# Kernel optimization log

Measured on AMD Instinct MI355X. Metric: run time of the kernel, lower is better.

The kernel has to match this reference:

```python
import jax, jax.numpy as jnp
import numpy as np

HIDDEN = 1024
N_HEAD = 16
D_HEAD = HIDDEN // N_HEAD


def setup_inputs() -> dict:
    key = jax.random.key(0)
    ks = jax.random.split(key, 12)
    B, S, H = 2, 2048, HIDDEN
    scale = 1.0 / np.sqrt(H)
    inp = {
        "q": jax.random.normal(ks[0], (B, S, H), jnp.float32),
        "k": jax.random.normal(ks[1], (B, S, H), jnp.float32),
        "v": jax.random.normal(ks[2], (B, S, H), jnp.float32),
        "mask": jnp.ones((B, 1, S, S), jnp.int32),
        "w_q": jax.random.normal(ks[3], (H, H), jnp.float32) * scale,
        "b_q": jnp.zeros((H,), jnp.float32),
        "w_k": jax.random.normal(ks[4], (H, H), jnp.float32) * scale,
        "b_k": jnp.zeros((H,), jnp.float32),
        "w_v": jax.random.normal(ks[5], (H, H), jnp.float32) * scale,
        "b_v": jnp.zeros((H,), jnp.float32),
        "w_o": jax.random.normal(ks[6], (H, H), jnp.float32) * scale,
        "b_o": jnp.zeros((H,), jnp.float32),
    }
    return inp


def reference(q, k, v, mask, w_q, b_q, w_k, b_k, w_v, b_v, w_o, b_o):
    B, Sq, H = q.shape
    Sk = k.shape[1]
    # projections (weights stored as [in, out])
    qh = (q @ w_q + b_q).reshape(B, Sq, N_HEAD, D_HEAD).transpose(0, 2, 1, 3)
    kh = (k @ w_k + b_k).reshape(B, Sk, N_HEAD, D_HEAD).transpose(0, 2, 1, 3)
    vh = (v @ w_v + b_v).reshape(B, Sk, N_HEAD, D_HEAD).transpose(0, 2, 1, 3)
    scores = jnp.einsum("bhqd,bhkd->bhqk", qh, kh) * (D_HEAD ** -0.5)
    scores = jnp.where(mask == 0, jnp.float32(-10000.0), scores)
    attn = jax.nn.softmax(scores, axis=-1)
    out = jnp.einsum("bhqk,bhkd->bhqd", attn, vh)
    out = out.transpose(0, 2, 1, 3).reshape(B, Sq, H)
    return out @ w_o + b_o
```

## Files before the change

kernel.cpp:

```cpp
#include <hip/hip_runtime.h>
#include <hip/hip_bf16.h>
#include <stdint.h>

#define S_LEN 2048
#define HID   1024
#define NHEAD 16
#define DHEAD 64
#define BATCH 2

#define QSCALE 0.18033688f
#define MASKNEG -14427.0f

typedef __bf16 bf16_t;
typedef __bf16 bf16x4 __attribute__((ext_vector_type(4)));
typedef __bf16 bf16x8 __attribute__((ext_vector_type(8)));
typedef float  f32x4  __attribute__((ext_vector_type(4)));

__device__ __forceinline__ void gl_lds16(const bf16_t* g, bf16_t* l) {
  __builtin_amdgcn_global_load_lds((const __attribute__((address_space(1))) void*)g,
                                   (__attribute__((address_space(3))) void*)l,
                                   16, 0, 0);
}

template<int TR, int TC>
__device__ __forceinline__ void stage_tile(const bf16_t* __restrict__ g, int ldg,
                                           bf16_t* lds, int wave, int lane) {
  constexpr int CH = TC / 8;
  constexpr int NINST = (TR * CH) / 64;
  #pragma unroll
  for (int i = wave; i < NINST; i += 4) {
    int slot = i * 64 + lane;
    int r  = slot / CH;
    int cs = slot & (CH - 1);
    int c  = cs ^ (r & (CH - 1));
    gl_lds16(g + (size_t)r * ldg + c * 8, lds + i * 512);
  }
}

template<int CH>
__device__ __forceinline__ bf16x8 frag_ld(const bf16_t* lds, int row, int kchunk) {
  int cs = kchunk ^ (row & (CH - 1));
  return *(const bf16x8*)(lds + (row * CH + cs) * 8);
}

__global__ __launch_bounds__(256) void cvt3(const float* __restrict__ q,
                                            const float* __restrict__ k,
                                            const float* __restrict__ v,
                                            bf16_t* __restrict__ qb,
                                            bf16_t* __restrict__ kb,
                                            bf16_t* __restrict__ vb) {
  int which = blockIdx.y;
  const float* src = which == 0 ? q : which == 1 ? k : v;
  bf16_t* dst = which == 0 ? qb : which == 1 ? kb : vb;
  size_t i = ((size_t)blockIdx.x * 256 + threadIdx.x) * 4;
  float4 u = *(const float4*)(src + i);
  bf16x4 o = {(bf16_t)u.x, (bf16_t)u.y, (bf16_t)u.z, (bf16_t)u.w};
  *(bf16x4*)(dst + i) = o;
}

__global__ __launch_bounds__(256) void transpose_w4(
    const float* __restrict__ w0, const float* __restrict__ w1,
    const float* __restrict__ w2, const float* __restrict__ w3,
    bf16_t* __restrict__ wt) {
  __shared__ float t[64][65];
  const float* W = blockIdx.z == 0 ? w0 : blockIdx.z == 1 ? w1 : blockIdx.z == 2 ? w2 : w3;
  bf16_t* WT = wt + (size_t)blockIdx.z * HID * HID;
  int tx = threadIdx.x & 63, ty = threadIdx.x >> 6;
  int r0 = blockIdx.y * 64, c0 = blockIdx.x * 64;
  #pragma unroll
  for (int i = ty; i < 64; i += 4) t[i][tx] = W[(size_t)(r0 + i) * HID + c0 + tx];
  __syncthreads();
  #pragma unroll
  for (int i = ty; i < 64; i += 4) WT[(size_t)(c0 + i) * HID + r0 + tx] = (bf16_t)t[tx][i];
}

__global__ __launch_bounds__(256) void mask_flags(const int* __restrict__ mask,
                                                  unsigned char* __restrict__ flags) {
  int kt = blockIdx.x, qtile = blockIdx.y, b = blockIdx.z;
  const int* base = mask + (size_t)b * S_LEN * S_LEN + (size_t)(qtile * 128) * S_LEN + kt * 128;
  int tid = threadIdx.x;
  int r = tid >> 1, half = tid & 1;
  const int4* p = (const int4*)(base + (size_t)r * S_LEN + half * 64);
  int ok = 1;
  #pragma unroll
  for (int i = 0; i < 16; ++i) {
    int4 u = p[i];
    ok &= (u.x != 0) & (u.y != 0) & (u.z != 0) & (u.w != 0);
  }
  __shared__ int anyz;
  if (tid == 0) anyz = 0;
  __syncthreads();
  if (!ok) atomicOr(&anyz, 1);
  __syncthreads();
  if (tid == 0) flags[(b * 16 + qtile) * 16 + kt] = anyz ? 0 : 1;
}

__global__ __launch_bounds__(256) void qkv_gemm(
    const bf16_t* __restrict__ qb, const bf16_t* __restrict__ kb, const bf16_t* __restrict__ vb,
    const bf16_t* __restrict__ wT,
    const float* __restrict__ bq, const float* __restrict__ bk, const float* __restrict__ bv,
    bf16_t* __restrict__ Qh, bf16_t* __restrict__ Kh, bf16_t* __restrict__ VhT) {
  int mode = blockIdx.z;
  const bf16_t* A    = mode == 0 ? qb : mode == 1 ? kb : vb;
  const bf16_t* Bt   = wT + (size_t)mode * HID * HID;
  const float*  bias = mode == 0 ? bq : mode == 1 ? bk : bv;

  __shared__ __align__(16) bf16_t As[128 * 64];
  __shared__ __align__(16) bf16_t Bs[128 * 64];

  int tid = threadIdx.x, wave = tid >> 6, lane = tid & 63;
  int lane15 = lane & 15, quad = lane >> 4;
  int m0 = blockIdx.x * 128, n0 = blockIdx.y * 128;
  int wm = (wave >> 1) * 64, wn = (wave & 1) * 64;

  f32x4 zero4 = {0.f, 0.f, 0.f, 0.f};
  f32x4 acc[4][4];
  #pragma unroll
  for (int t = 0; t < 4; ++t)
    #pragma unroll
    for (int n = 0; n < 4; ++n) acc[t][n] = zero4;

  for (int k0 = 0; k0 < HID; k0 += 64) {
    stage_tile<128, 64>(A  + (size_t)m0 * HID + k0, HID, As, wave, lane);
    stage_tile<128, 64>(Bt + (size_t)n0 * HID + k0, HID, Bs, wave, lane);
    __syncthreads();
    #pragma unroll
    for (int kc = 0; kc < 2; ++kc) {
      bf16x8 af[4], bfr[4];
      #pragma unroll
      for (int t = 0; t < 4; ++t) af[t]  = frag_ld<8>(As, wm + t * 16 + lane15, kc * 4 + quad);
      #pragma unroll
      for (int n = 0; n < 4; ++n) bfr[n] = frag_ld<8>(Bs, wn + n * 16 + lane15, kc * 4 + quad);
      if (mode < 2) {
        #pragma unroll
        for (int t = 0; t < 4; ++t)
          #pragma unroll
          for (int n = 0; n < 4; ++n)
            acc[t][n] = __builtin_amdgcn_mfma_f32_16x16x32_bf16(af[t], bfr[n], acc[t][n], 0, 0, 0);
      } else {
        #pragma unroll
        for (int t = 0; t < 4; ++t)
          #pragma unroll
          for (int n = 0; n < 4; ++n)
            acc[t][n] = __builtin_amdgcn_mfma_f32_16x16x32_bf16(bfr[n], af[t], acc[t][n], 0, 0, 0);
      }
    }
    __syncthreads();
  }

  if (mode < 2) {
    float sc = (mode == 0) ? QSCALE : 1.0f;
    bf16_t* dst = (mode == 0 ? Qh : Kh);
    #pragma unroll
    for (int t = 0; t < 4; ++t) {
      #pragma unroll
      for (int n = 0; n < 4; ++n) {
        int col = n0 + wn + n * 16 + lane15;
        float bb = bias[col];
        #pragma unroll
        for (int i = 0; i < 4; ++i) {
          int row = m0 + wm + t * 16 + quad * 4 + i;
          bf16_t o = (bf16_t)((acc[t][n][i] + bb) * sc);
          int b = row >> 11, s = row & 2047;
          int h = col >> 6,  d = col & 63;
          dst[((size_t)(b * NHEAD + h) * S_LEN + s) * DHEAD + d] = o;
        }
      }
    }
  } else {
    #pragma unroll
    for (int n = 0; n < 4; ++n) {
      int dbase = n0 + wn + n * 16 + quad * 4;
      float4 bb4 = *(const float4*)(bias + dbase);
      #pragma unroll
      for (int t = 0; t < 4; ++t) {
        int token = m0 + wm + t * 16 + lane15;
        int b = token >> 11, s = token & 2047;
        #pragma unroll
        for (int i = 0; i < 4; ++i) {
          int dg = dbase + i;
          int h = dg >> 6, d = dg & 63;
          float bb = i == 0 ? bb4.x : i == 1 ? bb4.y : i == 2 ? bb4.z : bb4.w;
          VhT[((size_t)(b * NHEAD + h) * DHEAD + d) * S_LEN + s] = (bf16_t)(acc[t][n][i] + bb);
        }
      }
    }
  }
}

__global__ __launch_bounds__(256) void attn_kernel(
    const bf16_t* __restrict__ Qh, const bf16_t* __restrict__ Kh, const bf16_t* __restrict__ VhT,
    const int* __restrict__ mask, const unsigned char* __restrict__ flags,
    bf16_t* __restrict__ O) {
  __shared__ __align__(16) bf16_t Ks[128 * 64];
  __shared__ __align__(16) bf16_t VTs[80 * 128];
  __shared__ __align__(16) bf16_t Ps[128 * 128];

  int tid = threadIdx.x, wave = tid >> 6, lane = tid & 63;
  int lane15 = lane & 15, quad = lane >> 4;
  int bh = blockIdx.y, b = bh >> 4, h = bh & 15;
  int qt = blockIdx.x;
  int wrow = wave * 32;

  if (tid < 128) VTs[64 * 128 + tid] = (bf16_t)1.0f;

  stage_tile<128, 64>(Qh + ((size_t)bh * S_LEN + qt * 128) * DHEAD, DHEAD, Ps, wave, lane);
  __syncthreads();
  bf16x8 qa[2][2];
  #pragma unroll
  for (int kc = 0; kc < 2; ++kc)
    #pragma unroll
    for (int nq = 0; nq < 2; ++nq)
      qa[kc][nq] = frag_ld<8>(Ps, wrow + nq * 16 + lane15, kc * 4 + quad);

  f32x4 zero4 = {0.f, 0.f, 0.f, 0.f};
  f32x4 o_acc[2][5];
  #pragma unroll
  for (int nq = 0; nq < 2; ++nq)
    #pragma unroll
    for (int mt = 0; mt < 5; ++mt) o_acc[nq][mt] = zero4;

  for (int kt = 0; kt < S_LEN / 128; ++kt) {
    stage_tile<128, 64>(Kh + ((size_t)bh * S_LEN + kt * 128) * DHEAD, DHEAD, Ks, wave, lane);
    stage_tile<64, 128>(VhT + (size_t)bh * DHEAD * S_LEN + kt * 128, S_LEN, VTs, wave, lane);
    __syncthreads();

    f32x4 sa[2][8];
    #pragma unroll
    for (int nq = 0; nq < 2; ++nq)
      #pragma unroll
      for (int mc = 0; mc < 8; ++mc) sa[nq][mc] = zero4;
    #pragma unroll
    for (int kc = 0; kc < 2; ++kc) {
      bf16x8 kf[8];
      #pragma unroll
      for (int mc = 0; mc < 8; ++mc) kf[mc] = frag_ld<8>(Ks, mc * 16 + lane15, kc * 4 + quad);
      #pragma unroll
      for (int nq = 0; nq < 2; ++nq)
        #pragma unroll
        for (int mc = 0; mc < 8; ++mc)
          sa[nq][mc] = __builtin_amdgcn_mfma_f32_16x16x32_bf16(kf[mc], qa[kc][nq], sa[nq][mc], 0, 0, 0);
    }

    if (flags[(b * 16 + qt) * 16 + kt] == 0) {
      #pragma unroll
      for (int nq = 0; nq < 2; ++nq)
        #pragma unroll
        for (int mc = 0; mc < 8; ++mc)
          #pragma unroll
          for (int i = 0; i < 4; ++i) {
            int q = qt * 128 + wrow + nq * 16 + lane15;
            int c = kt * 128 + mc * 16 + quad * 4 + i;
            if (mask[(size_t)b * S_LEN * S_LEN + (size_t)q * S_LEN + c] == 0)
              sa[nq][mc][i] = MASKNEG;
          }
    }

    #pragma unroll
    for (int nq = 0; nq < 2; ++nq) {
      int q = wrow + nq * 16 + lane15;
      #pragma unroll
      for (int mc = 0; mc < 8; ++mc) {
        bf16x4 pk = {(bf16_t)exp2f(sa[nq][mc][0]), (bf16_t)exp2f(sa[nq][mc][1]),
                     (bf16_t)exp2f(sa[nq][mc][2]), (bf16_t)exp2f(sa[nq][mc][3])};
        int chunk = mc * 2 + (quad >> 1);
        int slot = chunk ^ (q & 15);
        *(bf16x4*)(Ps + q * 128 + slot * 8 + (quad & 1) * 4) = pk;
      }
    }

    #pragma unroll
    for (int kc = 0; kc < 4; ++kc) {
      bf16x8 vf[5], pf[2];
      #pragma unroll
      for (int mt = 0; mt < 5; ++mt) vf[mt] = frag_ld<16>(VTs, mt * 16 + lane15, kc * 4 + quad);
      #pragma unroll
      for (int nq = 0; nq < 2; ++nq) pf[nq] = frag_ld<16>(Ps, wrow + nq * 16 + lane15, kc * 4 + quad);
      #pragma unroll
      for (int nq = 0; nq < 2; ++nq)
        #pragma unroll
        for (int mt = 0; mt < 5; ++mt)
          o_acc[nq][mt] = __builtin_amdgcn_mfma_f32_16x16x32_bf16(vf[mt], pf[nq], o_acc[nq][mt], 0, 0, 0);
    }
    __syncthreads();
  }

  #pragma unroll
  for (int nq = 0; nq < 2; ++nq) {
    float lval = __shfl(o_acc[nq][4][0], lane15);
    float inv = 1.0f / lval;
    int s = qt * 128 + wrow + nq * 16 + lane15;
    size_t orow = ((size_t)b * S_LEN + s) * HID + h * DHEAD;
    #pragma unroll
    for (int mt = 0; mt < 4; ++mt) {
      bf16x4 ov = {(bf16_t)(o_acc[nq][mt][0] * inv), (bf16_t)(o_acc[nq][mt][1] * inv),
                   (bf16_t)(o_acc[nq][mt][2] * inv), (bf16_t)(o_acc[nq][mt][3] * inv)};
      *(bf16x4*)(O + orow + mt * 16 + quad * 4) = ov;
    }
  }
}

__global__ __launch_bounds__(256) void oproj_gemm(
    const bf16_t* __restrict__ A, const bf16_t* __restrict__ Bt,
    const float* __restrict__ bias, float* __restrict__ out) {
  __shared__ __align__(16) bf16_t As[128 * 64];
  __shared__ __align__(16) bf16_t Bs[128 * 64];

  int tid = threadIdx.x, wave = tid >> 6, lane = tid & 63;
  int lane15 = lane & 15, quad = lane >> 4;
  int m0 = blockIdx.x * 128, n0 = blockIdx.y * 128;
  int wm = (wave >> 1) * 64, wn = (wave & 1) * 64;

  f32x4 zero4 = {0.f, 0.f, 0.f, 0.f};
  f32x4 acc[4][4];
  #pragma unroll
  for (int t = 0; t < 4; ++t)
    #pragma unroll
    for (int n = 0; n < 4; ++n) acc[t][n] = zero4;

  for (int k0 = 0; k0 < HID; k0 += 64) {
    stage_tile<128, 64>(A  + (size_t)m0 * HID + k0, HID, As, wave, lane);
    stage_tile<128, 64>(Bt + (size_t)n0 * HID + k0, HID, Bs, wave, lane);
    __syncthreads();
    #pragma unroll
    for (int kc = 0; kc < 2; ++kc) {
      bf16x8 af[4], bfr[4];
      #pragma unroll
      for (int t = 0; t < 4; ++t) af[t]  = frag_ld<8>(As, wm + t * 16 + lane15, kc * 4 + quad);
      #pragma unroll
      for (int n = 0; n < 4; ++n) bfr[n] = frag_ld<8>(Bs, wn + n * 16 + lane15, kc * 4 + quad);
      #pragma unroll
      for (int t = 0; t < 4; ++t)
        #pragma unroll
        for (int n = 0; n < 4; ++n)
          acc[t][n] = __builtin_amdgcn_mfma_f32_16x16x32_bf16(af[t], bfr[n], acc[t][n], 0, 0, 0);
    }
    __syncthreads();
  }

  #pragma unroll
  for (int t = 0; t < 4; ++t) {
    #pragma unroll
    for (int n = 0; n < 4; ++n) {
      int col = n0 + wn + n * 16 + lane15;
      float bb = bias[col];
      #pragma unroll
      for (int i = 0; i < 4; ++i) {
        int row = m0 + wm + t * 16 + quad * 4 + i;
        out[(size_t)row * HID + col] = acc[t][n][i] + bb;
      }
    }
  }
}

extern "C" void kernel_launch(void* const* d_in, const int* in_sizes, int n_in,
                              void* d_out, int out_size, void* d_ws, size_t ws_size,
                              hipStream_t stream) {
  (void)in_sizes; (void)n_in; (void)out_size; (void)ws_size;
  const float* q  = (const float*)d_in[0];
  const float* k  = (const float*)d_in[1];
  const float* v  = (const float*)d_in[2];
  const int*  mask = (const int*)d_in[3];
  const float* wq = (const float*)d_in[4];
  const float* bq = (const float*)d_in[5];
  const float* wk = (const float*)d_in[6];
  const float* bk = (const float*)d_in[7];
  const float* wv = (const float*)d_in[8];
  const float* bv = (const float*)d_in[9];
  const float* wo = (const float*)d_in[10];
  const float* bo = (const float*)d_in[11];

  char* ws = (char*)d_ws;
  bf16_t* wT    = (bf16_t*)(ws);
  bf16_t* Qh    = (bf16_t*)(ws + (8u  << 20));
  bf16_t* Kh    = (bf16_t*)(ws + (16u << 20));
  bf16_t* VhT   = (bf16_t*)(ws + (24u << 20));
  bf16_t* qb    = (bf16_t*)(ws + (32u << 20));
  bf16_t* kb    = (bf16_t*)(ws + (40u << 20));
  bf16_t* vb    = (bf16_t*)(ws + (48u << 20));
  unsigned char* flags = (unsigned char*)(ws + (56u << 20));
  bf16_t* Obuf  = qb;

  cvt3<<<dim3(4096, 3), 256, 0, stream>>>(q, k, v, qb, kb, vb);
  transpose_w4<<<dim3(16, 16, 4), 256, 0, stream>>>(wq, wk, wv, wo, wT);
  mask_flags<<<dim3(16, 16, 2), 256, 0, stream>>>(mask, flags);
  qkv_gemm<<<dim3(32, 8, 3), 256, 0, stream>>>(qb, kb, vb, wT, bq, bk, bv, Qh, Kh, VhT);
  attn_kernel<<<dim3(16, 32), 256, 0, stream>>>(Qh, Kh, VhT, mask, flags, Obuf);
  oproj_gemm<<<dim3(32, 8), 256, 0, stream>>>(Obuf, wT + (size_t)3 * HID * HID, bo, (float*)d_out);
}
```

Before: 279.6 us.

## Split attention over two key halves and merge partials in a combine kernel

The attention kernel now splits the key sequence into two halves along a new grid dimension. This doubles the number of blocks and writes unnormalized partial outputs and row sums, which a new combine kernel adds together and normalizes. The inner loop now processes keys in 32-column quarters with a smaller P buffer, and row sums come from register accumulation instead of a ones-column MFMA. This shrinks LDS and register footprint so launch_bounds can request higher occupancy. In exchange it adds an extra kernel launch and a round trip through global memory for the partial results.

```diff
diff --git a/kernel.cpp b/kernel.cpp
--- a/kernel.cpp
+++ b/kernel.cpp
@@ -188,98 +188,106 @@
   }
 }
 
-__global__ __launch_bounds__(256) void attn_kernel(
+__global__ __launch_bounds__(256, 4) void attn_kernel(
     const bf16_t* __restrict__ Qh, const bf16_t* __restrict__ Kh, const bf16_t* __restrict__ VhT,
     const int* __restrict__ mask, const unsigned char* __restrict__ flags,
-    bf16_t* __restrict__ O) {
+    bf16_t* __restrict__ OP, float* __restrict__ LP) {
   __shared__ __align__(16) bf16_t Ks[128 * 64];
-  __shared__ __align__(16) bf16_t VTs[80 * 128];
-  __shared__ __align__(16) bf16_t Ps[128 * 128];
+  __shared__ __align__(16) bf16_t VTs[64 * 128];
+  __shared__ __align__(16) bf16_t Ps[128 * 32];
 
   int tid = threadIdx.x, wave = tid >> 6, lane = tid & 63;
   int lane15 = lane & 15, quad = lane >> 4;
-  int bh = blockIdx.y, b = bh >> 4, h = bh & 15;
+  int bh = blockIdx.y, b = bh >> 4;
   int qt = blockIdx.x;
+  int half = blockIdx.z;
   int wrow = wave * 32;
 
-  if (tid < 128) VTs[64 * 128 + tid] = (bf16_t)1.0f;
-
-  stage_tile<128, 64>(Qh + ((size_t)bh * S_LEN + qt * 128) * DHEAD, DHEAD, Ps, wave, lane);
+  stage_tile<128, 64>(Qh + ((size_t)bh * S_LEN + qt * 128) * DHEAD, DHEAD, Ks, wave, lane);
   __syncthreads();
   bf16x8 qa[2][2];
   #pragma unroll
   for (int kc = 0; kc < 2; ++kc)
     #pragma unroll
     for (int nq = 0; nq < 2; ++nq)
-      qa[kc][nq] = frag_ld<8>(Ps, wrow + nq * 16 + lane15, kc * 4 + quad);
+      qa[kc][nq] = frag_ld<8>(Ks, wrow + nq * 16 + lane15, kc * 4 + quad);
+  __syncthreads();
 
   f32x4 zero4 = {0.f, 0.f, 0.f, 0.f};
-  f32x4 o_acc[2][5];
+  f32x4 o_acc[2][4];
+  float l_acc[2] = {0.f, 0.f};
   #pragma unroll
   for (int nq = 0; nq < 2; ++nq)
     #pragma unroll
-    for (int mt = 0; mt < 5; ++mt) o_acc[nq][mt] = zero4;
-
-  for (int kt = 0; kt < S_LEN / 128; ++kt) {
+    for (int mt = 0; mt < 4; ++mt) o_acc[nq][mt] = zero4;
+
+  for (int ktl = 0; ktl < 8; ++ktl) {
+    int kt = half * 8 + ktl;
     stage_tile<128, 64>(Kh + ((size_t)bh * S_LEN + kt * 128) * DHEAD, DHEAD, Ks, wave, lane);
     stage_tile<64, 128>(VhT + (size_t)bh * DHEAD * S_LEN + kt * 128, S_LEN, VTs, wave, lane);
     __syncthreads();
-
-    f32x4 sa[2][8];
-    #pragma unroll
-    for (int nq = 0; nq < 2; ++nq)
-      #pragma unroll
-      for (int mc = 0; mc < 8; ++mc) sa[nq][mc] = zero4;
-    #pragma unroll
-    for (int kc = 0; kc < 2; ++kc) {
-      bf16x8 kf[8];
-      #pragma unroll
-      for (int mc = 0; mc < 8; ++mc) kf[mc] = frag_ld<8>(Ks, mc * 16 + lane15, kc * 4 + quad);
+    bool masked = flags[(b * 16 + qt) * 16 + kt] == 0;
+
+    #pragma unroll
+    for (int qtr = 0; qtr < 4; ++qtr) {
+      f32x4 sa[2][2];
       #pragma unroll
       for (int nq = 0; nq < 2; ++nq)
         #pragma unroll
-        for (int mc = 0; mc < 8; ++mc)
-          sa[nq][mc] = __builtin_amdgcn_mfma_f32_16x16x32_bf16(kf[mc], qa[kc][nq], sa[nq][mc], 0, 0, 0);
-    }
-
-    if (flags[(b * 16 + qt) * 16 + kt] == 0) {
+        for (int mc = 0; mc < 2; ++mc) sa[nq][mc] = zero4;
+      #pragma unroll
+      for (int kc = 0; kc < 2; ++kc) {
+        bf16x8 kf[2];
+        #pragma unroll
+        for (int mc = 0; mc < 2; ++mc)
+          kf[mc] = frag_ld<8>(Ks, qtr * 32 + mc * 16 + lane15, kc * 4 + quad);
+        #pragma unroll
+        for (int nq = 0; nq < 2; ++nq)
+          #pragma unroll
+          for (int mc = 0; mc < 2; ++mc)
+            sa[nq][mc] = __builtin_amdgcn_mfma_f32_16x16x32_bf16(kf[mc], qa[kc][nq], sa[nq][mc], 0, 0, 0);
+      }
+
+      if (masked) {
+        #pragma unroll
+        for (int nq = 0; nq < 2; ++nq)
+          #pragma unroll
+          for (int mc = 0; mc < 2; ++mc)
+            #pragma unroll
+            for (int i = 0; i < 4; ++i) {
+              int q = qt * 128 + wrow + nq * 16 + lane15;
+              int c = kt * 128 + qtr * 32 + mc * 16 + quad * 4 + i;
+              if (mask[(size_t)b * S_LEN * S_LEN + (size_t)q * S_LEN + c] == 0)
+                sa[nq][mc][i] = MASKNEG;
+            }
+      }
+
+      #pragma unroll
+      for (int nq = 0; nq < 2; ++nq) {
+        int q = wrow + nq * 16 + lane15;
+        #pragma unroll
+        for (int mc = 0; mc < 2; ++mc) {
+          float e0 = exp2f(sa[nq][mc][0]), e1 = exp2f(sa[nq][mc][1]);
+          float e2 = exp2f(sa[nq][mc][2]), e3 = exp2f(sa[nq][mc][3]);
+          l_acc[nq] += (e0 + e1) + (e2 + e3);
+          bf16x4 pk = {(bf16_t)e0, (bf16_t)e1, (bf16_t)e2, (bf16_t)e3};
+          int chunk = mc * 2 + (quad >> 1);
+          int slot = chunk ^ (q & 3);
+          *(bf16x4*)(Ps + q * 32 + slot * 8 + (quad & 1) * 4) = pk;
+        }
+      }
+
+      bf16x8 vf[4], pf[2];
+      #pragma unroll
+      for (int mt = 0; mt < 4; ++mt)
+        vf[mt] = frag_ld<16>(VTs, mt * 16 + lane15, qtr * 4 + quad);
       #pragma unroll
       for (int nq = 0; nq < 2; ++nq)
-        #pragma unroll
-        for (int mc = 0; mc < 8; ++mc)
-          #pragma unroll
-          for (int i = 0; i < 4; ++i) {
-            int q = qt * 128 + wrow + nq * 16 + lane15;
-            int c = kt * 128 + mc * 16 + quad * 4 + i;
-            if (mask[(size_t)b * S_LEN * S_LEN + (size_t)q * S_LEN + c] == 0)
-              sa[nq][mc][i] = MASKNEG;
-          }
-    }
-
-    #pragma unroll
-    for (int nq = 0; nq < 2; ++nq) {
-      int q = wrow + nq * 16 + lane15;
-      #pragma unroll
-      for (int mc = 0; mc < 8; ++mc) {
-        bf16x4 pk = {(bf16_t)exp2f(sa[nq][mc][0]), (bf16_t)exp2f(sa[nq][mc][1]),
-                     (bf16_t)exp2f(sa[nq][mc][2]), (bf16_t)exp2f(sa[nq][mc][3])};
-        int chunk = mc * 2 + (quad >> 1);
-        int slot = chunk ^ (q & 15);
-        *(bf16x4*)(Ps + q * 128 + slot * 8 + (quad & 1) * 4) = pk;
-      }
-    }
-
-    #pragma unroll
-    for (int kc = 0; kc < 4; ++kc) {
-      bf16x8 vf[5], pf[2];
-      #pragma unroll
-      for (int mt = 0; mt < 5; ++mt) vf[mt] = frag_ld<16>(VTs, mt * 16 + lane15, kc * 4 + quad);
-      #pragma unroll
-      for (int nq = 0; nq < 2; ++nq) pf[nq] = frag_ld<16>(Ps, wrow + nq * 16 + lane15, kc * 4 + quad);
+        pf[nq] = frag_ld<4>(Ps, wrow + nq * 16 + lane15, quad);
       #pragma unroll
       for (int nq = 0; nq < 2; ++nq)
         #pragma unroll
-        for (int mt = 0; mt < 5; ++mt)
+        for (int mt = 0; mt < 4; ++mt)
           o_acc[nq][mt] = __builtin_amdgcn_mfma_f32_16x16x32_bf16(vf[mt], pf[nq], o_acc[nq][mt], 0, 0, 0);
     }
     __syncthreads();
@@ -287,17 +295,37 @@
 
   #pragma unroll
   for (int nq = 0; nq < 2; ++nq) {
-    float lval = __shfl(o_acc[nq][4][0], lane15);
-    float inv = 1.0f / lval;
+    float lv = l_acc[nq];
+    lv += __shfl_xor(lv, 16);
+    lv += __shfl_xor(lv, 32);
     int s = qt * 128 + wrow + nq * 16 + lane15;
-    size_t orow = ((size_t)b * S_LEN + s) * HID + h * DHEAD;
+    size_t obase = (size_t)(half * 32 + bh) * S_LEN + s;
     #pragma unroll
     for (int mt = 0; mt < 4; ++mt) {
-      bf16x4 ov = {(bf16_t)(o_acc[nq][mt][0] * inv), (bf16_t)(o_acc[nq][mt][1] * inv),
-                   (bf16_t)(o_acc[nq][mt][2] * inv), (bf16_t)(o_acc[nq][mt][3] * inv)};
-      *(bf16x4*)(O + orow + mt * 16 + quad * 4) = ov;
-    }
-  }
+      bf16x4 ov = {(bf16_t)o_acc[nq][mt][0], (bf16_t)o_acc[nq][mt][1],
+                   (bf16_t)o_acc[nq][mt][2], (bf16_t)o_acc[nq][mt][3]};
+      *(bf16x4*)(OP + obase * 64 + mt * 16 + quad * 4) = ov;
+    }
+    if (quad == 0) LP[obase] = lv;
+  }
+}
+
+__global__ __launch_bounds__(256) void attn_combine(
+    const bf16_t* __restrict__ OP, const float* __restrict__ LP,
+    bf16_t* __restrict__ O) {
+  int bh = blockIdx.y, b = bh >> 4, h = bh & 15;
+  int s = blockIdx.x * 32 + (threadIdx.x >> 3);
+  int d0 = (threadIdx.x & 7) * 8;
+  size_t i0 = (size_t)bh * S_LEN + s;
+  size_t i1 = (size_t)(32 + bh) * S_LEN + s;
+  bf16x8 a = *(const bf16x8*)(OP + i0 * 64 + d0);
+  bf16x8 c = *(const bf16x8*)(OP + i1 * 64 + d0);
+  float inv = 1.0f / (LP[i0] + LP[i1]);
+  bf16x8 o;
+  #pragma unroll
+  for (int j = 0; j < 8; ++j)
+    o[j] = (bf16_t)(((float)a[j] + (float)c[j]) * inv);
+  *(bf16x8*)(O + ((size_t)b * S_LEN + s) * HID + h * DHEAD + d0) = o;
 }
 
 __global__ __launch_bounds__(256) void oproj_gemm(
@@ -379,12 +407,15 @@
   bf16_t* kb    = (bf16_t*)(ws + (40u << 20));
   bf16_t* vb    = (bf16_t*)(ws + (48u << 20));
   unsigned char* flags = (unsigned char*)(ws + (56u << 20));
-  bf16_t* Obuf  = qb;
+  bf16_t* OP    = (bf16_t*)(ws + (32u << 20));
+  float*  LPx   = (float*)(ws + (48u << 20));
+  bf16_t* Obuf  = Qh;
 
   cvt3<<<dim3(4096, 3), 256, 0, stream>>>(q, k, v, qb, kb, vb);
   transpose_w4<<<dim3(16, 16, 4), 256, 0, stream>>>(wq, wk, wv, wo, wT);
   mask_flags<<<dim3(16, 16, 2), 256, 0, stream>>>(mask, flags);
   qkv_gemm<<<dim3(32, 8, 3), 256, 0, stream>>>(qb, kb, vb, wT, bq, bk, bv, Qh, Kh, VhT);
-  attn_kernel<<<dim3(16, 32), 256, 0, stream>>>(Qh, Kh, VhT, mask, flags, Obuf);
+  attn_kernel<<<dim3(16, 32, 2), 256, 0, stream>>>(Qh, Kh, VhT, mask, flags, OP, LPx);
+  attn_combine<<<dim3(64, 32), 256, 0, stream>>>(OP, LPx, Obuf);
   oproj_gemm<<<dim3(32, 8), 256, 0, stream>>>(Obuf, wT + (size_t)3 * HID * HID, bo, (float*)d_out);
 }
```

Result: slower. 339.7 us (+21.5%).

## Fuse fp32-to-bf16 input conversion into QKV GEMM staging and restructure mask scan

Applied to the files above, without the earlier changes.

Removes the separate cvt3 kernel. The QKV GEMM now loads fp32 activations directly, converts them to bf16 in registers and writes them into the swizzled LDS tile, which removes one launch and the bf16 intermediate round trip. The trade-off is that the A-tile staging is now a synchronous register path instead of global_load_lds, and each fp32 A tile is re-read by all N blocks at twice the bytes. Separately, mask_flags is rewritten to launch only 32 blocks, each scanning a full 128-row strip across all key tiles, which cuts block count but greatly reduces parallelism for reading the large mask.

```diff
diff --git a/kernel.cpp b/kernel.cpp
--- a/kernel.cpp
+++ b/kernel.cpp
@@ -37,25 +37,28 @@
   }
 }
 
+template<int TR>
+__device__ __forceinline__ void stage_cvt_tile(const float* __restrict__ g, int ldg,
+                                               bf16_t* lds, int tid) {
+  constexpr int NSLOT = TR * 8;
+  #pragma unroll
+  for (int i = 0; i < NSLOT / 256; ++i) {
+    int slot = i * 256 + tid;
+    int r  = slot >> 3;
+    int cs = slot & 7;
+    int c  = cs ^ (r & 7);
+    const float4* src = (const float4*)(g + (size_t)r * ldg + c * 8);
+    float4 u0 = src[0], u1 = src[1];
+    bf16x8 o = {(bf16_t)u0.x, (bf16_t)u0.y, (bf16_t)u0.z, (bf16_t)u0.w,
+                (bf16_t)u1.x, (bf16_t)u1.y, (bf16_t)u1.z, (bf16_t)u1.w};
+    *(bf16x8*)(lds + slot * 8) = o;
+  }
+}
+
 template<int CH>
 __device__ __forceinline__ bf16x8 frag_ld(const bf16_t* lds, int row, int kchunk) {
   int cs = kchunk ^ (row & (CH - 1));
   return *(const bf16x8*)(lds + (row * CH + cs) * 8);
-}
-
-__global__ __launch_bounds__(256) void cvt3(const float* __restrict__ q,
-                                            const float* __restrict__ k,
-                                            const float* __restrict__ v,
-                                            bf16_t* __restrict__ qb,
-                                            bf16_t* __restrict__ kb,
-                                            bf16_t* __restrict__ vb) {
-  int which = blockIdx.y;
-  const float* src = which == 0 ? q : which == 1 ? k : v;
-  bf16_t* dst = which == 0 ? qb : which == 1 ? kb : vb;
-  size_t i = ((size_t)blockIdx.x * 256 + threadIdx.x) * 4;
-  float4 u = *(const float4*)(src + i);
-  bf16x4 o = {(bf16_t)u.x, (bf16_t)u.y, (bf16_t)u.z, (bf16_t)u.w};
-  *(bf16x4*)(dst + i) = o;
 }
 
 __global__ __launch_bounds__(256) void transpose_w4(
@@ -76,32 +79,32 @@
 
 __global__ __launch_bounds__(256) void mask_flags(const int* __restrict__ mask,
                                                   unsigned char* __restrict__ flags) {
-  int kt = blockIdx.x, qtile = blockIdx.y, b = blockIdx.z;
-  const int* base = mask + (size_t)b * S_LEN * S_LEN + (size_t)(qtile * 128) * S_LEN + kt * 128;
+  int qtile = blockIdx.x, b = blockIdx.y;
+  const int* base = mask + (size_t)b * S_LEN * S_LEN + (size_t)(qtile * 128) * S_LEN;
   int tid = threadIdx.x;
-  int r = tid >> 1, half = tid & 1;
-  const int4* p = (const int4*)(base + (size_t)r * S_LEN + half * 64);
+  int kt = tid >> 4;
   int ok = 1;
-  #pragma unroll
-  for (int i = 0; i < 16; ++i) {
-    int4 u = p[i];
-    ok &= (u.x != 0) & (u.y != 0) & (u.z != 0) & (u.w != 0);
-  }
-  __shared__ int anyz;
-  if (tid == 0) anyz = 0;
+  for (int r = 0; r < 128; ++r) {
+    const int4* p = (const int4*)(base + (size_t)r * S_LEN + tid * 8);
+    int4 a = p[0], c = p[1];
+    ok &= (a.x != 0) & (a.y != 0) & (a.z != 0) & (a.w != 0) &
+          (c.x != 0) & (c.y != 0) & (c.z != 0) & (c.w != 0);
+  }
+  __shared__ int oks[16];
+  if (tid < 16) oks[tid] = 1;
   __syncthreads();
-  if (!ok) atomicOr(&anyz, 1);
+  if (!ok) atomicAnd(&oks[kt], 0);
   __syncthreads();
-  if (tid == 0) flags[(b * 16 + qtile) * 16 + kt] = anyz ? 0 : 1;
+  if (tid < 16) flags[(b * 16 + qtile) * 16 + tid] = (unsigned char)oks[tid];
 }
 
 __global__ __launch_bounds__(256) void qkv_gemm(
-    const bf16_t* __restrict__ qb, const bf16_t* __restrict__ kb, const bf16_t* __restrict__ vb,
+    const float* __restrict__ qf, const float* __restrict__ kf32, const float* __restrict__ vf32,
     const bf16_t* __restrict__ wT,
     const float* __restrict__ bq, const float* __restrict__ bk, const float* __restrict__ bv,
     bf16_t* __restrict__ Qh, bf16_t* __restrict__ Kh, bf16_t* __restrict__ VhT) {
   int mode = blockIdx.z;
-  const bf16_t* A    = mode == 0 ? qb : mode == 1 ? kb : vb;
+  const float*  A    = mode == 0 ? qf : mode == 1 ? kf32 : vf32;
   const bf16_t* Bt   = wT + (size_t)mode * HID * HID;
   const float*  bias = mode == 0 ? bq : mode == 1 ? bk : bv;
 
@@ -121,7 +124,7 @@
     for (int n = 0; n < 4; ++n) acc[t][n] = zero4;
 
   for (int k0 = 0; k0 < HID; k0 += 64) {
-    stage_tile<128, 64>(A  + (size_t)m0 * HID + k0, HID, As, wave, lane);
+    stage_cvt_tile<128>(A + (size_t)m0 * HID + k0, HID, As, tid);
     stage_tile<128, 64>(Bt + (size_t)n0 * HID + k0, HID, Bs, wave, lane);
     __syncthreads();
     #pragma unroll
@@ -375,16 +378,12 @@
   bf16_t* Qh    = (bf16_t*)(ws + (8u  << 20));
   bf16_t* Kh    = (bf16_t*)(ws + (16u << 20));
   bf16_t* VhT   = (bf16_t*)(ws + (24u << 20));
-  bf16_t* qb    = (bf16_t*)(ws + (32u << 20));
-  bf16_t* kb    = (bf16_t*)(ws + (40u << 20));
-  bf16_t* vb    = (bf16_t*)(ws + (48u << 20));
-  unsigned char* flags = (unsigned char*)(ws + (56u << 20));
-  bf16_t* Obuf  = qb;
-
-  cvt3<<<dim3(4096, 3), 256, 0, stream>>>(q, k, v, qb, kb, vb);
+  bf16_t* Obuf  = (bf16_t*)(ws + (32u << 20));
+  unsigned char* flags = (unsigned char*)(ws + (40u << 20));
+
   transpose_w4<<<dim3(16, 16, 4), 256, 0, stream>>>(wq, wk, wv, wo, wT);
-  mask_flags<<<dim3(16, 16, 2), 256, 0, stream>>>(mask, flags);
-  qkv_gemm<<<dim3(32, 8, 3), 256, 0, stream>>>(qb, kb, vb, wT, bq, bk, bv, Qh, Kh, VhT);
+  mask_flags<<<dim3(16, 2), 256, 0, stream>>>(mask, flags);
+  qkv_gemm<<<dim3(32, 8, 3), 256, 0, stream>>>(q, k, v, wT, bq, bk, bv, Qh, Kh, VhT);
   attn_kernel<<<dim3(16, 32), 256, 0, stream>>>(Qh, Kh, VhT, mask, flags, Obuf);
   oproj_gemm<<<dim3(32, 8), 256, 0, stream>>>(Obuf, wT + (size_t)3 * HID * HID, bo, (float*)d_out);
 }
```

After: 315.5 us. 1.13x slower.
